# Optimization experiments

Measured on AMD Instinct MI355X. Metric: run time of the kernel, lower is better.

## Reference

```python
import jax, jax.numpy as jnp
import numpy as np

B, C, L, M, EMB, HID = 32, 64, 8192, 32, 256, 64

def setup_inputs() -> dict:
    key = jax.random.key(0)
    ks = jax.random.split(key, 14)
    s_w = 1.0 / (C * C)
    s_a = 1.0 / EMB
    return {
        "x": jax.random.normal(ks[0], (B, C, L), jnp.float32),
        "emb": jax.random.normal(ks[1], (B, EMB), jnp.float32),
        "weights_pos": s_w * jax.random.normal(ks[2], (C, C, M, 2), jnp.float32),
        "weights_neg": s_w * jax.random.normal(ks[3], (C, C, M, 2), jnp.float32),
        "A_real_pos": s_a * jax.random.normal(ks[4], (M, EMB), jnp.float32),
        "A_imag_pos": s_a * jax.random.normal(ks[5], (M, EMB), jnp.float32),
        "A_real_neg": s_a * jax.random.normal(ks[6], (M, EMB), jnp.float32),
        "A_imag_neg": s_a * jax.random.normal(ks[7], (M, EMB), jnp.float32),
        "tm_w1": 0.05 * jax.random.normal(ks[8], (HID, EMB), jnp.float32),
        "tm_b1": jnp.zeros((HID,), jnp.float32),
        "tm_w2": 0.05 * jax.random.normal(ks[9], (2 * C, HID), jnp.float32),
        "tm_b2": jnp.zeros((2 * C,), jnp.float32),
        "lin_w": 0.05 * jax.random.normal(ks[10], (C, C), jnp.float32),
        "lin_b": jnp.zeros((C,), jnp.float32),
    }

def reference(x, emb, weights_pos, weights_neg, A_real_pos, A_imag_pos,
              A_real_neg, A_imag_neg, tm_w1, tm_b1, tm_w2, tm_b2, lin_w, lin_b):
    b, c, l = x.shape
    m = weights_pos.shape[2]
    k = l // 2 + 1
    # ---- SpectralConv1d branch ----
    x_ft = jnp.fft.rfft(x, norm="ortho")  # [B,C,K] complex
    wp = weights_pos[..., 0] + 1j * weights_pos[..., 1]  # [Ci,Co,M]
    wn = weights_neg[..., 0] + 1j * weights_neg[..., 1]
    phi_p = (emb @ A_real_pos.T) + 1j * (emb @ A_imag_pos.T)  # [B,M]
    phi_n = (emb @ A_real_neg.T) + 1j * (emb @ A_imag_neg.T)
    out_pos = jnp.einsum("bim,iom->bom", x_ft[:, :, :m], wp) * phi_p[:, None, :]
    out_neg = jnp.einsum("bim,iom->bom", x_ft[:, :, k - m:], wn) * phi_n[:, None, :]
    out_ft = jnp.zeros((b, c, k), dtype=x_ft.dtype)
    out_ft = out_ft.at[:, :, :m].set(out_pos).at[:, :, k - m:].set(out_neg)
    x1 = jnp.fft.irfft(out_ft, n=l, norm="ortho")  # [B,C,L]
    # ---- Conv1DTime branch (FiLM-style) ----
    h = jax.nn.silu(emb @ tm_w1.T + tm_b1)          # [B,HID]
    gb = h @ tm_w2.T + tm_b2                         # [B,2C]
    gamma, beta = gb[:, :c], gb[:, c:]
    xl = jnp.einsum("bcl,oc->bol", x, lin_w) + lin_b[None, :, None]
    x2 = xl * (1.0 + gamma[:, :, None]) + beta[:, :, None]
    return jax.nn.silu(x1 + x2)
```

## Files before the change

kernel.cpp:

```cpp
#include <hip/hip_runtime.h>
#include <math.h>

#define L_ 8192
#define EMB_ 256
#define HID_ 64

typedef __attribute__((ext_vector_type(8))) short bf16x8;
typedef __attribute__((ext_vector_type(4))) float f32x4;
typedef __attribute__((ext_vector_type(4))) int i32x4;

#define OFF_TFB  0
#define OFF_TLB  262144
#define OFF_AFB  524288
#define OFF_XFRP 917504
#define OFF_B2   3014656
#define OFF_PHI  3016704
#define OFF_GB   3020800
#define OFF_WT   3024896
#define OFF_XT   3549184

__device__ inline int pkbf(float a, float b) {
    int r;
    asm volatile("v_cvt_pk_bf16_f32 %0, %1, %2" : "=v"(r) : "v"(a), "v"(b));
    return r;
}
__device__ inline bf16x8 asbf(i32x4 v) { union { i32x4 i; bf16x8 h; } u; u.i = v; return u.h; }
#define MFMA(A,B,C) __builtin_amdgcn_mfma_f32_16x16x32_bf16((A),(B),(C),0,0,0)

__device__ inline ushort f2bf(float v) {
    unsigned b = __float_as_uint(v);
    return (ushort)((b + 0x7FFFu + ((b >> 16) & 1u)) >> 16);
}
__device__ inline float bf2f(ushort h) { return __uint_as_float(((unsigned)h) << 16); }
__device__ inline float hwsin(float rev) { float r; asm("v_sin_f32 %0, %1" : "=v"(r) : "v"(rev)); return r; }
__device__ inline float hwcos(float rev) { float r; asm("v_cos_f32 %0, %1" : "=v"(r) : "v"(rev)); return r; }

__global__ __launch_bounds__(256) void k_init(ushort* __restrict__ TLB, ushort* __restrict__ TFB,
        const float* __restrict__ emb,
        const float* __restrict__ Arp, const float* __restrict__ Aip,
        const float* __restrict__ Arn, const float* __restrict__ Ain, float* __restrict__ phi,
        const float* __restrict__ w1, const float* __restrict__ b1,
        const float* __restrict__ w2, const float* __restrict__ b2, float* __restrict__ gb,
        const float* __restrict__ wpos, const float* __restrict__ wneg, float* __restrict__ WT) {
    int bid = blockIdx.x;
    if (bid < 4096) {
        int idx = bid * 256 + threadIdx.x;
        int f, l; ushort* dst;
        if (idx < 524288) {
            int u = idx;
            int e = u & 7, lane = (u >> 3) & 63, ct = (u >> 9) & 3, kstep = u >> 11;
            l = kstep * 32 + ((lane >> 4) << 3) + e;
            f = ct * 16 + (lane & 15);
            dst = TLB + u;
        } else {
            int u = idx - 524288;
            int e = u & 7, lane = (u >> 3) & 63, ts = (u >> 9) & 1, lt = u >> 10;
            l = lt * 16 + (lane & 15);
            f = ts * 32 + ((lane >> 4) << 3) + e;
            dst = TFB + u;
        }
        int fr = f & 31; bool sinp = (f & 32) != 0;
        int r = (fr * l) & (L_ - 1);
        float rev = (float)r * (1.0f / (float)L_);
        float v = sinp ? hwsin(rev) : hwcos(rev);
        *dst = f2bf(v);
    } else if (bid < 4112) {
        int tid = (bid - 4096) * 256 + threadIdx.x;
        int b = tid >> 7;
        int mm = (tid >> 2) & 31;
        int cmp = tid & 3;
        const float* A = (cmp == 0) ? Arp : (cmp == 1) ? Aip : (cmp == 2) ? Arn : Ain;
        const float4* e4 = (const float4*)(emb + b * EMB_);
        const float4* a4 = (const float4*)(A + mm * EMB_);
        float acc = 0.f;
        for (int q = 0; q < EMB_ / 4; ++q) {
            float4 ev = e4[q], av = a4[q];
            acc += ev.x * av.x + ev.y * av.y + ev.z * av.z + ev.w * av.w;
        }
        phi[tid] = acc;
    } else if (bid < 4144) {
        __shared__ float h[HID_];
        int b = bid - 4112, t = threadIdx.x;
        if (t < HID_) {
            const float4* e4 = (const float4*)(emb + b * EMB_);
            const float4* w4 = (const float4*)(w1 + t * EMB_);
            float acc = b1[t];
            for (int q = 0; q < EMB_ / 4; ++q) {
                float4 ev = e4[q], wv = w4[q];
                acc += ev.x * wv.x + ev.y * wv.y + ev.z * wv.z + ev.w * wv.w;
            }
            h[t] = acc / (1.f + expf(-acc));
        }
        __syncthreads();
        if (t < 128) {
            float g = b2[t];
            const float4* h4 = (const float4*)h;
            const float4* w4 = (const float4*)(w2 + t * HID_);
            for (int q = 0; q < HID_ / 4; ++q) {
                float4 hv = h4[q], wv = w4[q];
                g += hv.x * wv.x + hv.y * wv.y + hv.z * wv.z + hv.w * wv.w;
            }
            if (t < 64) gb[(b * 64 + t) * 2 + 0] = 1.f + g;
            else        gb[(b * 64 + (t - 64)) * 2 + 1] = g;
        }
    } else {
        int t = bid - 4144;
        int side = t >> 6, i = t & 63;
        const float* W = side ? wneg : wpos;
        const float* src = W + (size_t)i * 4096;
        int tid = threadIdx.x;
        #pragma unroll
        for (int j = 0; j < 8; ++j) {
            int u = tid + 256 * j;
            int mm = u >> 6, o = u & 63;
            float2 v = *(const float2*)(src + o * 64 + mm * 2);
            *(float2*)(WT + ((size_t)(side * 32 + mm)) * 8192 + i * 128 + o * 2) = v;
        }
    }
}

__global__ __launch_bounds__(256) void k_dft(const float* __restrict__ x,
        const ushort* __restrict__ TLB, float* __restrict__ xfrp, ushort* __restrict__ XT) {
    __shared__ float sP[4][16][132];
    int stripe = blockIdx.x >> 3;
    int lseg = blockIdx.x & 7;
    int w = threadIdx.x >> 6;
    int lane = threadIdx.x & 63;
    int row = lane & 15, koff = (lane >> 4) << 3;
    int r0 = stripe * 16;
    int kb0 = lseg * 1024 + w * 256;

    f32x4 acc[8];
    #pragma unroll
    for (int i = 0; i < 8; ++i) acc[i] = (f32x4){0.f, 0.f, 0.f, 0.f};

    const float* ap = x + (size_t)(r0 + row) * L_ + kb0 + koff;
    const i32x4* tb = (const i32x4*)TLB;
    int tbase = (kb0 >> 5) * 256 + lane;
    const i32x4 SM = {(int)0x80000000, (int)0x80000000, (int)0x80000000, (int)0x80000000};

    float4 xa0 = *(const float4*)(ap);
    float4 xc0 = *(const float4*)(ap + 4);
    float4 xa1 = *(const float4*)(ap + 32);
    float4 xc1 = *(const float4*)(ap + 36);
    float4 xa2 = *(const float4*)(ap + 64);
    float4 xc2 = *(const float4*)(ap + 68);
    i32x4 t0 = tb[tbase], t1 = tb[tbase + 64], t2 = tb[tbase + 128], t3 = tb[tbase + 192];
    #pragma unroll
    for (int ks = 0; ks < 8; ++ks) {
        float4 nxa = {0,0,0,0}, nxc = {0,0,0,0};
        i32x4 n0 = t0, n1 = t1, n2 = t2, n3 = t3;
        if (ks < 5) {
            nxa = *(const float4*)(ap + (ks + 3) * 32);
            nxc = *(const float4*)(ap + (ks + 3) * 32 + 4);
        }
        if (ks < 7) {
            int ti = tbase + (ks + 1) * 256;
            n0 = tb[ti]; n1 = tb[ti + 64]; n2 = tb[ti + 128]; n3 = tb[ti + 192];
        }
        int h0 = pkbf(xa0.x, xa0.y), h1 = pkbf(xa0.z, xa0.w);
        int h2 = pkbf(xc0.x, xc0.y), h3 = pkbf(xc0.z, xc0.w);
        bf16x8 AH = asbf((i32x4){h0, h1, h2, h3});
        {
            ushort* xtp = XT + (((size_t)stripe * 8192 + kb0 + koff + ks * 32) << 4) + row;
            xtp[0]   = (ushort)h0;  xtp[16]  = (ushort)((unsigned)h0 >> 16);
            xtp[32]  = (ushort)h1;  xtp[48]  = (ushort)((unsigned)h1 >> 16);
            xtp[64]  = (ushort)h2;  xtp[80]  = (ushort)((unsigned)h2 >> 16);
            xtp[96]  = (ushort)h3;  xtp[112] = (ushort)((unsigned)h3 >> 16);
        }
        acc[0] = MFMA(AH, asbf(t0), acc[0]); acc[4] = MFMA(AH, asbf(t0 ^ SM), acc[4]);
        acc[1] = MFMA(AH, asbf(t1), acc[1]); acc[5] = MFMA(AH, asbf(t1 ^ SM), acc[5]);
        acc[2] = MFMA(AH, asbf(t2), acc[2]); acc[6] = MFMA(AH, asbf(t2 ^ SM), acc[6]);
        acc[3] = MFMA(AH, asbf(t3), acc[3]); acc[7] = MFMA(AH, asbf(t3 ^ SM), acc[7]);
        xa0 = xa1; xc0 = xc1; xa1 = xa2; xc1 = xc2; xa2 = nxa; xc2 = nxc;
        t0 = n0; t1 = n1; t2 = n2; t3 = n3;
    }
    int crow = (lane >> 4) << 2;
    int ccol = lane & 15;
    #pragma unroll
    for (int ct = 0; ct < 8; ++ct)
        #pragma unroll
        for (int r = 0; r < 4; ++r)
            sP[w][crow + r][ct * 16 + ccol] = acc[ct][r];
    __syncthreads();
    #pragma unroll
    for (int i = 0; i < 8; ++i) {
        int e = threadIdx.x + 256 * i;
        int rr = e & 15, cc = e >> 4;
        float s = sP[0][rr][cc] + sP[1][rr][cc] + sP[2][rr][cc] + sP[3][rr][cc];
        xfrp[((size_t)(lseg * 128 + cc)) * 2048 + r0 + rr] = s;
    }
}

__global__ __launch_bounds__(256) void k_mix(const float* __restrict__ xfrt,
        const float* __restrict__ WT,
        const float* __restrict__ phi, const float* __restrict__ lw,
        const float* __restrict__ lb, const float* __restrict__ gb,
        ushort* __restrict__ afb, float* __restrict__ bias2) {
    int bi = blockIdx.x;
    int tid = threadIdx.x;
    if (bi >= 256) {
        int b = bi - 256;
        ushort* dst = afb + (size_t)b * 24576;
        #pragma unroll
        for (int j = 0; j < 16; ++j) {
            int u = tid + 256 * j;
            int e = u & 7, lane = (u >> 3) & 63, mt = (u >> 9) & 3, ks2 = u >> 11;
            int c = mt * 16 + (lane & 15);
            int kk = ((lane >> 4) << 3) + e;
            float v = lw[c * 64 + ks2 * 32 + kk] * gb[(b * 64 + c) * 2];
            ushort hi = f2bf(v);
            int base = (((4 + ks2) * 4 + mt) * 64 + lane) * 16;
            dst[base + e] = hi;
            dst[base + 8 + e] = f2bf(v - bf2f(hi));
        }
        if (tid < 64) {
            float g1 = gb[(b * 64 + tid) * 2], be = gb[(b * 64 + tid) * 2 + 1];
            bias2[b * 64 + tid] = lb[tid] * g1 + be;
        }
        return;
    }
    __shared__ float sW[64][64][2];
    __shared__ float sXr[8][64], sXi[8][64];
    int bh = bi & 3, side = (bi >> 2) & 1, mm = bi >> 3;
    int slot = side ? (31 - mm) : mm;
    int colR = side ? (64 + slot) : mm;
    int colI = side ? (96 + slot) : (32 + mm);

    {
        const float4* wt = (const float4*)(WT + ((size_t)(side * 32 + mm)) * 8192);
        float* sWlin = &sW[0][0][0];
        #pragma unroll
        for (int j = 0; j < 8; ++j) {
            int u = tid + 256 * j;
            *(float4*)&sWlin[u * 4] = wt[u];
        }
    }
    {
        const float2* pR = (const float2*)(xfrt + (size_t)colR * 2048 + bh * 512);
        const float2* pI = (const float2*)(xfrt + (size_t)colI * 2048 + bh * 512);
        float2 aR = {0, 0}, aI = {0, 0};
        #pragma unroll
        for (int s = 0; s < 8; ++s) {
            float2 vR = pR[(size_t)s * 131072 + tid];
            float2 vI = pI[(size_t)s * 131072 + tid];
            aR.x += vR.x; aR.y += vR.y;
            aI.x += vI.x; aI.y += vI.y;
        }
        if (!side) { aI.x = -aI.x; aI.y = -aI.y; }
        *(float2*)&sXr[tid >> 5][(tid & 31) * 2] = aR;
        *(float2*)&sXi[tid >> 5][(tid & 31) * 2] = aI;
    }
    __syncthreads();

    int o = tid & 63, bg = tid >> 6;
    const float invL = 1.f / (float)L_;
    float fac = (slot == 0) ? invL : 2.f * invL;
    int comp = side ? 2 : 0;
    int e = slot & 7, kgrp = slot >> 3;
    int mt = o >> 4, lane = kgrp * 16 + (o & 15);
    #pragma unroll
    for (int bl = 0; bl < 2; ++bl) {
        int b_local = bg * 2 + bl;
        int b = bh * 8 + b_local;
        float sre = 0.f, sim = 0.f;
        #pragma unroll 16
        for (int i = 0; i < 64; ++i) {
            float wr = sW[i][o][0], wi = sW[i][o][1];
            float xr = sXr[b_local][i], xi = sXi[b_local][i];
            sre += xr * wr - xi * wi;
            sim += xr * wi + xi * wr;
        }
        const float* ph = &phi[(b * 32 + mm) * 4 + (side ? 2 : 0)];
        float phr = ph[0], phim = ph[1];
        float Pre = sre * phr - sim * phim;
        float Pim = sre * phim + sim * phr;
        float a = fac * Pre;
        float bcoef = (slot == 0) ? 0.f : (side ? 2.f * invL * Pim : -2.f * invL * Pim);
        ushort* dst = afb + (size_t)b * 24576;
        ushort hiA = f2bf(a);
        int baseA = ((comp * 4 + mt) * 64 + lane) * 16;
        dst[baseA + e] = hiA;
        dst[baseA + 8 + e] = f2bf(a - bf2f(hiA));
        ushort hiB = f2bf(bcoef);
        int baseB = (((comp + 1) * 4 + mt) * 64 + lane) * 16;
        dst[baseB + e] = hiB;
        dst[baseB + 8 + e] = f2bf(bcoef - bf2f(hiB));
    }
}

#define TPART(ts)                                                                        \
    {                                                                                    \
        i32x4 bh_[2];                                                                    \
        _Pragma("unroll")                                                                \
        for (int nj = 0; nj < 2; ++nj)                                                   \
            bh_[nj] = tb[((lt0 + nj) * 2 + (ts)) * 64 + lane];                           \
        _Pragma("unroll")                                                                \
        for (int mt = 0; mt < 4; ++mt) {                                                 \
            i32x4 ah0 = ab[(((ts) * 4 + mt) * 64 + lane) * 2];                           \
            i32x4 ah1 = ab[(((2 + (ts)) * 4 + mt) * 64 + lane) * 2];                     \
            bf16x8 AH0 = asbf(ah0), AH1 = asbf(ah1);                                     \
            _Pragma("unroll")                                                            \
            for (int nj = 0; nj < 2; ++nj) {                                             \
                acc[mt][nj] = MFMA(AH0, asbf(bh_[nj]), acc[mt][nj]);                     \
                acc[mt][nj] = MFMA(AH1, asbf(bh_[nj] ^ SM), acc[mt][nj]);                \
            }                                                                            \
        }                                                                                \
    }

#define XPART(ts, xv0, xv1)                                                              \
    {                                                                                    \
        bf16x8 XH0 = asbf(xv0), XH1 = asbf(xv1);                                         \
        _Pragma("unroll")                                                                \
        for (int mt = 0; mt < 4; ++mt) {                                                 \
            i32x4 ah = ab[(((4 + (ts)) * 4 + mt) * 64 + lane) * 2];                      \
            bf16x8 AH = asbf(ah);                                                        \
            acc[mt][0] = MFMA(AH, XH0, acc[mt][0]);                                      \
            acc[mt][1] = MFMA(AH, XH1, acc[mt][1]);                                      \
        }                                                                                \
    }

__global__ __launch_bounds__(256, 3) void k_fuse(const ushort* __restrict__ XT,
        const ushort* __restrict__ TFB, const ushort* __restrict__ AFB,
        const float* __restrict__ bias2, float* __restrict__ out) {
    int b = blockIdx.x >> 6, lt = blockIdx.x & 63;
    int w = threadIdx.x >> 6, lane = threadIdx.x & 63;
    int col = lane & 15, kgrp = lane >> 4;
    int lbase = lt * 128 + w * 32;
    int lt0 = lbase >> 4;
    const i32x4* tb = (const i32x4*)TFB;
    const i32x4* ab = (const i32x4*)AFB + (size_t)b * 3072;
    const i32x4* xt = (const i32x4*)XT;

    f32x4 acc[4][2];
    #pragma unroll
    for (int i = 0; i < 4; ++i)
        #pragma unroll
        for (int j = 0; j < 2; ++j) acc[i][j] = (f32x4){0.f, 0.f, 0.f, 0.f};

    int sm = (col & 1) ? (int)0x80008000 : 0;
    i32x4 SM = {sm, sm, sm, sm};

    size_t xs0 = ((size_t)(b * 4 + (kgrp >> 1)) * 8192 + lbase + col) * 2 + (kgrp & 1);
    size_t xs1 = ((size_t)(b * 4 + 2 + (kgrp >> 1)) * 8192 + lbase + col) * 2 + (kgrp & 1);
    i32x4 xv00 = xt[xs0];
    i32x4 xv01 = xt[xs0 + 32];
    i32x4 xv10 = xt[xs1];
    i32x4 xv11 = xt[xs1 + 32];

    TPART(0)
    XPART(0, xv00, xv01)
    TPART(1)
    XPART(1, xv10, xv11)

    #pragma unroll
    for (int mt = 0; mt < 4; ++mt) {
        #pragma unroll
        for (int r = 0; r < 4; ++r) {
            int c = mt * 16 + kgrp * 4 + r;
            float bias = bias2[b * 64 + c];
            float* op = out + (size_t)(b * 64 + c) * L_ + lbase + col;
            #pragma unroll
            for (int nj = 0; nj < 2; ++nj) {
                float v = acc[mt][nj][r] + bias;
                op[nj * 16] = v / (1.f + __expf(-v));
            }
        }
    }
}

extern "C" void kernel_launch(void* const* d_in, const int* in_sizes, int n_in,
                              void* d_out, int out_size, void* d_ws, size_t ws_size,
                              hipStream_t stream) {
    const float* x    = (const float*)d_in[0];
    const float* emb  = (const float*)d_in[1];
    const float* wpos = (const float*)d_in[2];
    const float* wneg = (const float*)d_in[3];
    const float* Arp  = (const float*)d_in[4];
    const float* Aip  = (const float*)d_in[5];
    const float* Arn  = (const float*)d_in[6];
    const float* Ain  = (const float*)d_in[7];
    const float* w1   = (const float*)d_in[8];
    const float* b1   = (const float*)d_in[9];
    const float* w2   = (const float*)d_in[10];
    const float* b2   = (const float*)d_in[11];
    const float* lw   = (const float*)d_in[12];
    const float* lb   = (const float*)d_in[13];
    float* out = (float*)d_out;
    float* ws = (float*)d_ws;
    ushort* TFB  = (ushort*)(ws + OFF_TFB);
    ushort* TLB  = (ushort*)(ws + OFF_TLB);
    ushort* AFB  = (ushort*)(ws + OFF_AFB);
    float*  XFRP = ws + OFF_XFRP;
    float*  B2   = ws + OFF_B2;
    float*  PHI  = ws + OFF_PHI;
    float*  GB   = ws + OFF_GB;
    float*  WT   = ws + OFF_WT;
    ushort* XT   = (ushort*)(ws + OFF_XT);

    hipLaunchKernelGGL(k_init,  dim3(4272), dim3(256), 0, stream,
                       TLB, TFB, emb, Arp, Aip, Arn, Ain, PHI, w1, b1, w2, b2, GB,
                       wpos, wneg, WT);
    hipLaunchKernelGGL(k_dft,   dim3(1024), dim3(256), 0, stream, x, TLB, XFRP, XT);
    hipLaunchKernelGGL(k_mix,   dim3(288),  dim3(256), 0, stream, XFRP, WT, PHI,
                       lw, lb, GB, AFB, B2);
    hipLaunchKernelGGL(k_fuse,  dim3(2048), dim3(256), 0, stream, XT, TFB, AFB, B2, out);
}
```

Measured before the change: 67.51 us.

## Store bf16 x transpose as packed 32-bit pairs and deepen twiddle prefetch

```diff
diff --git a/kernel.cpp b/kernel.cpp
--- a/kernel.cpp
+++ b/kernel.cpp
@@ -34,6 +34,11 @@
 __device__ inline float bf2f(ushort h) { return __uint_as_float(((unsigned)h) << 16); }
 __device__ inline float hwsin(float rev) { float r; asm("v_sin_f32 %0, %1" : "=v"(r) : "v"(rev)); return r; }
 __device__ inline float hwcos(float rev) { float r; asm("v_cos_f32 %0, %1" : "=v"(r) : "v"(rev)); return r; }
+__device__ inline unsigned permb(unsigned hi, unsigned lo, unsigned sel) {
+    unsigned r;
+    asm("v_perm_b32 %0, %1, %2, %3" : "=v"(r) : "v"(hi), "v"(lo), "v"(sel));
+    return r;
+}
 
 __global__ __launch_bounds__(256) void k_init(ushort* __restrict__ TLB, ushort* __restrict__ TFB,
         const float* __restrict__ emb,
@@ -119,8 +124,8 @@
     }
 }
 
-__global__ __launch_bounds__(256) void k_dft(const float* __restrict__ x,
-        const ushort* __restrict__ TLB, float* __restrict__ xfrp, ushort* __restrict__ XT) {
+__global__ __launch_bounds__(256, 4) void k_dft(const float* __restrict__ x,
+        const ushort* __restrict__ TLB, float* __restrict__ xfrp, unsigned* __restrict__ XT2) {
     __shared__ float sP[4][16][132];
     int stripe = blockIdx.x >> 3;
     int lseg = blockIdx.x & 7;
@@ -138,6 +143,7 @@
     const i32x4* tb = (const i32x4*)TLB;
     int tbase = (kb0 >> 5) * 256 + lane;
     const i32x4 SM = {(int)0x80000000, (int)0x80000000, (int)0x80000000, (int)0x80000000};
+    unsigned* xtb = XT2 + ((size_t)stripe * 4096 + ((kb0 + koff) >> 1)) * 16 + row;
 
     float4 xa0 = *(const float4*)(ap);
     float4 xc0 = *(const float4*)(ap + 4);
@@ -146,34 +152,36 @@
     float4 xa2 = *(const float4*)(ap + 64);
     float4 xc2 = *(const float4*)(ap + 68);
     i32x4 t0 = tb[tbase], t1 = tb[tbase + 64], t2 = tb[tbase + 128], t3 = tb[tbase + 192];
+    i32x4 u0 = tb[tbase + 256], u1 = tb[tbase + 320], u2 = tb[tbase + 384], u3 = tb[tbase + 448];
     #pragma unroll
     for (int ks = 0; ks < 8; ++ks) {
         float4 nxa = {0,0,0,0}, nxc = {0,0,0,0};
-        i32x4 n0 = t0, n1 = t1, n2 = t2, n3 = t3;
+        i32x4 v0 = u0, v1 = u1, v2 = u2, v3 = u3;
         if (ks < 5) {
             nxa = *(const float4*)(ap + (ks + 3) * 32);
             nxc = *(const float4*)(ap + (ks + 3) * 32 + 4);
         }
-        if (ks < 7) {
-            int ti = tbase + (ks + 1) * 256;
-            n0 = tb[ti]; n1 = tb[ti + 64]; n2 = tb[ti + 128]; n3 = tb[ti + 192];
+        if (ks < 6) {
+            int ti = tbase + (ks + 2) * 256;
+            v0 = tb[ti]; v1 = tb[ti + 64]; v2 = tb[ti + 128]; v3 = tb[ti + 192];
         }
         int h0 = pkbf(xa0.x, xa0.y), h1 = pkbf(xa0.z, xa0.w);
         int h2 = pkbf(xc0.x, xc0.y), h3 = pkbf(xc0.z, xc0.w);
         bf16x8 AH = asbf((i32x4){h0, h1, h2, h3});
-        {
-            ushort* xtp = XT + (((size_t)stripe * 8192 + kb0 + koff + ks * 32) << 4) + row;
-            xtp[0]   = (ushort)h0;  xtp[16]  = (ushort)((unsigned)h0 >> 16);
-            xtp[32]  = (ushort)h1;  xtp[48]  = (ushort)((unsigned)h1 >> 16);
-            xtp[64]  = (ushort)h2;  xtp[80]  = (ushort)((unsigned)h2 >> 16);
-            xtp[96]  = (ushort)h3;  xtp[112] = (ushort)((unsigned)h3 >> 16);
-        }
         acc[0] = MFMA(AH, asbf(t0), acc[0]); acc[4] = MFMA(AH, asbf(t0 ^ SM), acc[4]);
         acc[1] = MFMA(AH, asbf(t1), acc[1]); acc[5] = MFMA(AH, asbf(t1 ^ SM), acc[5]);
         acc[2] = MFMA(AH, asbf(t2), acc[2]); acc[6] = MFMA(AH, asbf(t2 ^ SM), acc[6]);
         acc[3] = MFMA(AH, asbf(t3), acc[3]); acc[7] = MFMA(AH, asbf(t3 ^ SM), acc[7]);
+        {
+            unsigned* xtp = xtb + (size_t)(ks * 16) * 16;
+            xtp[0]  = (unsigned)h0;
+            xtp[16] = (unsigned)h1;
+            xtp[32] = (unsigned)h2;
+            xtp[48] = (unsigned)h3;
+        }
         xa0 = xa1; xc0 = xc1; xa1 = xa2; xc1 = xc2; xa2 = nxa; xc2 = nxc;
-        t0 = n0; t1 = n1; t2 = n2; t3 = n3;
+        t0 = u0; t1 = u1; t2 = u2; t3 = u3;
+        u0 = v0; u1 = v1; u2 = v2; u3 = v3;
     }
     int crow = (lane >> 4) << 2;
     int ccol = lane & 15;
@@ -320,7 +328,14 @@
         }                                                                                \
     }
 
-__global__ __launch_bounds__(256, 3) void k_fuse(const ushort* __restrict__ XT,
+#define XEXTRACT(q0, q1, dstvar)                                                         \
+    dstvar = (i32x4){                                                                    \
+        (int)permb((unsigned)q0[1], (unsigned)q0[0], sel),                               \
+        (int)permb((unsigned)q0[3], (unsigned)q0[2], sel),                               \
+        (int)permb((unsigned)q1[1], (unsigned)q1[0], sel),                               \
+        (int)permb((unsigned)q1[3], (unsigned)q1[2], sel)};
+
+__global__ __launch_bounds__(256, 3) void k_fuse(const unsigned* __restrict__ XT2,
         const ushort* __restrict__ TFB, const ushort* __restrict__ AFB,
         const float* __restrict__ bias2, float* __restrict__ out) {
     int b = blockIdx.x >> 6, lt = blockIdx.x & 63;
@@ -330,7 +345,7 @@
     int lt0 = lbase >> 4;
     const i32x4* tb = (const i32x4*)TFB;
     const i32x4* ab = (const i32x4*)AFB + (size_t)b * 3072;
-    const i32x4* xt = (const i32x4*)XT;
+    const i32x4* xt4 = (const i32x4*)XT2;
 
     f32x4 acc[4][2];
     #pragma unroll
@@ -340,17 +355,26 @@
 
     int sm = (col & 1) ? (int)0x80008000 : 0;
     i32x4 SM = {sm, sm, sm, sm};
-
-    size_t xs0 = ((size_t)(b * 4 + (kgrp >> 1)) * 8192 + lbase + col) * 2 + (kgrp & 1);
-    size_t xs1 = ((size_t)(b * 4 + 2 + (kgrp >> 1)) * 8192 + lbase + col) * 2 + (kgrp & 1);
-    i32x4 xv00 = xt[xs0];
-    i32x4 xv01 = xt[xs0 + 32];
-    i32x4 xv10 = xt[xs1];
-    i32x4 xv11 = xt[xs1 + 32];
+    unsigned sel = (col & 1) ? 0x07060302u : 0x05040100u;
+
+    size_t i00 = ((size_t)(b * 4 + (kgrp >> 1)) * 4096 + ((lbase + col) >> 1)) * 4 + (kgrp & 1) * 2;
+    size_t i01 = i00 + 8 * 4;
+    size_t i10 = i00 + (size_t)2 * 4096 * 4;
+    size_t i11 = i10 + 8 * 4;
+    i32x4 q000 = xt4[i00], q001 = xt4[i00 + 1];
+    i32x4 q010 = xt4[i01], q011 = xt4[i01 + 1];
+    i32x4 q100 = xt4[i10], q101 = xt4[i10 + 1];
+    i32x4 q110 = xt4[i11], q111 = xt4[i11 + 1];
 
     TPART(0)
+    i32x4 xv00, xv01;
+    XEXTRACT(q000, q001, xv00)
+    XEXTRACT(q010, q011, xv01)
     XPART(0, xv00, xv01)
     TPART(1)
+    i32x4 xv10, xv11;
+    XEXTRACT(q100, q101, xv10)
+    XEXTRACT(q110, q111, xv11)
     XPART(1, xv10, xv11)
 
     #pragma unroll
@@ -388,21 +412,21 @@
     const float* lb   = (const float*)d_in[13];
     float* out = (float*)d_out;
     float* ws = (float*)d_ws;
-    ushort* TFB  = (ushort*)(ws + OFF_TFB);
-    ushort* TLB  = (ushort*)(ws + OFF_TLB);
-    ushort* AFB  = (ushort*)(ws + OFF_AFB);
-    float*  XFRP = ws + OFF_XFRP;
-    float*  B2   = ws + OFF_B2;
-    float*  PHI  = ws + OFF_PHI;
-    float*  GB   = ws + OFF_GB;
-    float*  WT   = ws + OFF_WT;
-    ushort* XT   = (ushort*)(ws + OFF_XT);
+    ushort*   TFB  = (ushort*)(ws + OFF_TFB);
+    ushort*   TLB  = (ushort*)(ws + OFF_TLB);
+    ushort*   AFB  = (ushort*)(ws + OFF_AFB);
+    float*    XFRP = ws + OFF_XFRP;
+    float*    B2   = ws + OFF_B2;
+    float*    PHI  = ws + OFF_PHI;
+    float*    GB   = ws + OFF_GB;
+    float*    WT   = ws + OFF_WT;
+    unsigned* XT2  = (unsigned*)(ws + OFF_XT);
 
     hipLaunchKernelGGL(k_init,  dim3(4272), dim3(256), 0, stream,
                        TLB, TFB, emb, Arp, Aip, Arn, Ain, PHI, w1, b1, w2, b2, GB,
                        wpos, wneg, WT);
-    hipLaunchKernelGGL(k_dft,   dim3(1024), dim3(256), 0, stream, x, TLB, XFRP, XT);
+    hipLaunchKernelGGL(k_dft,   dim3(1024), dim3(256), 0, stream, x, TLB, XFRP, XT2);
     hipLaunchKernelGGL(k_mix,   dim3(288),  dim3(256), 0, stream, XFRP, WT, PHI,
                        lw, lb, GB, AFB, B2);
-    hipLaunchKernelGGL(k_fuse,  dim3(2048), dim3(256), 0, stream, XT, TFB, AFB, B2, out);
-}
+    hipLaunchKernelGGL(k_fuse,  dim3(2048), dim3(256), 0, stream, XT2, TFB, AFB, B2, out);
+}
```

New measurement: 66.43 us. About the same (-1.6%).
